# Kernel optimization log

Hardware: AMD Instinct MI355X
Metric: run time of the kernel (lower is better)

Reference implementation:

```python
import jax, jax.numpy as jnp
import numpy as np

B, DIM, IN_DIM, H, W = 4, 256, 128, 128, 128
DD = IN_DIM // 2          # down_dim = 64
HEADS = 8
BN_EPS = 1e-5


def conv2d(x, w, b=None, pad=0, dil=1):
    y = jax.lax.conv_general_dilated(
        x, w, window_strides=(1, 1),
        padding=[(pad, pad), (pad, pad)],
        rhs_dilation=(dil, dil),
        dimension_numbers=('NCHW', 'OIHW', 'NCHW'))
    if b is not None:
        y = y + b[None, :, None, None]
    return y


def bn_relu(x, s, o):
    # eval-mode BatchNorm2d with running_mean=0, running_var=1
    return jax.nn.relu(x * (s / np.sqrt(1.0 + BN_EPS))[None, :, None, None] + o[None, :, None, None])


def setup_inputs() -> dict:
    ks = iter(jax.random.split(jax.random.key(0), 80))

    def w(shape, sc=0.05):
        return sc * jax.random.normal(next(ks), shape, jnp.float32)

    def s(c):
        return 1.0 + 0.1 * jax.random.normal(next(ks), (c,), jnp.float32)

    def o(c):
        return 0.02 * jax.random.normal(next(ks), (c,), jnp.float32)

    d = {}
    d['x'] = jax.random.normal(next(ks), (B, DIM, H, W), jnp.float32)
    d['w_dc'] = w((IN_DIM, DIM, 3, 3)); d['b_dc'] = w((IN_DIM,)); d['s_dc'] = s(IN_DIM); d['o_dc'] = o(IN_DIM)
    d['w1'] = w((DD, IN_DIM, 1, 1)); d['b1'] = w((DD,)); d['s1'] = s(DD); d['o1'] = o(DD)
    d['w2'] = w((DD, DD, 3, 3)); d['b2'] = w((DD,)); d['s2'] = s(DD); d['o2'] = o(DD)
    d['w3'] = w((DD, DD, 3, 3)); d['b3'] = w((DD,)); d['s3'] = s(DD); d['o3'] = o(DD)
    d['w4'] = w((DD, DD, 3, 3)); d['b4'] = w((DD,)); d['s4'] = s(DD); d['o4'] = o(DD)
    d['w5'] = w((DD, IN_DIM, 1, 1)); d['b5'] = w((DD,)); d['s5'] = s(DD); d['o5'] = o(DD)
    d['temperature'] = jnp.ones((HEADS, 1, 1), jnp.float32)
    d['w_po'] = w((DD, 2 * DD, 1, 1))  # project_out, bias=False
    d['w_wa'] = w((DD // 16, DD, 1, 1)); d['b_wa'] = w((DD // 16,)); d['s_wa'] = s(DD // 16); d['o_wa'] = o(DD // 16)
    d['w_wb'] = w((DD, DD // 16, 1, 1)); d['b_wb'] = w((DD,))
    d['w_f'] = w((DD, 5 * DD, 1, 1)); d['b_f'] = w((DD,)); d['s_f'] = s(DD); d['o_f'] = o(DD)
    d['w_oa'] = w((DD // 2, DD, 3, 3)); d['b_oa'] = w((DD // 2,)); d['s_oa'] = s(DD // 2); d['o_oa'] = o(DD // 2)
    d['w_ob'] = w((1, DD // 2, 1, 1)); d['b_ob'] = w((1,))
    return d


def reference(x, w_dc, b_dc, s_dc, o_dc, w1, b1, s1, o1, w2, b2, s2, o2,
              w3, b3, s3, o3, w4, b4, s4, o4, w5, b5, s5, o5,
              temperature, w_po, w_wa, b_wa, s_wa, o_wa, w_wb, b_wb,
              w_f, b_f, s_f, o_f, w_oa, b_oa, s_oa, o_oa, w_ob, b_ob):

    def branch(c):
        b, ch, h, wd = c.shape
        f = jnp.fft.fft2(c)                                   # [b,ch,h,w] complex64 (q=k=v=tepqkv)
        qkv = f.reshape(b, HEADS, ch // HEADS, h * wd)        # v (unnormalized)
        n = jnp.sqrt(jnp.sum(jnp.square(jnp.abs(qkv)), axis=-1, keepdims=True))
        qn = qkv / jnp.maximum(n, 1e-12)                      # F.normalize(dim=-1); q == k
        attn = jnp.einsum('bhcn,bhdn->bhcd', qn, qn) * temperature
        # custom complex normalization: separate real/imag softmax
        attn = jax.lax.complex(jax.nn.softmax(attn.real, axis=-1),
                               jax.nn.softmax(attn.imag, axis=-1))
        of = jnp.abs(jnp.fft.ifft2(jnp.einsum('bhcd,bhdn->bhcn', attn, qkv)))  # ifft2 over (c, hw)
        of = of.reshape(b, ch, h, wd)
        g = jax.nn.sigmoid(conv2d(bn_relu(conv2d(f.real, w_wa, b_wa), s_wa, o_wa), w_wb, b_wb))
        ol = jnp.abs(jnp.fft.ifft2(g * f))                    # ifft2 over (h, w)
        return conv2d(jnp.concatenate([of, ol], axis=1), w_po) + c

    xd = bn_relu(conv2d(x, w_dc, b_dc, pad=1), s_dc, o_dc)
    c1 = bn_relu(conv2d(xd, w1, b1), s1, o1)
    c2 = bn_relu(conv2d(c1, w2, b2, pad=3, dil=3), s2, o2)
    F2 = branch(c2)
    c3 = bn_relu(conv2d(c1 + F2, w3, b3, pad=5, dil=5), s3, o3)
    F3 = branch(c3)
    c4 = bn_relu(conv2d(c1 + F3, w4, b4, pad=7, dil=7), s4, o4)
    F4 = branch(c4)
    # conv5: global avg pool -> 1x1 conv -> bilinear upsample of a 1x1 map == broadcast
    c5 = bn_relu(conv2d(jnp.mean(xd, axis=(2, 3), keepdims=True), w5, b5), s5, o5)
    c5 = jnp.broadcast_to(c5, (c5.shape[0], c5.shape[1], xd.shape[2], xd.shape[3]))
    fused = bn_relu(conv2d(jnp.concatenate([c1, F2, F3, F4, c5], axis=1), w_f, b_f), s_f, o_f)
    return conv2d(bn_relu(conv2d(fused, w_oa, b_oa, pad=1), s_oa, o_oa), w_ob, b_ob)
```

## Files before the change

### kernel.cpp

```cpp
#include <hip/hip_runtime.h>

#define S 16384
#define PI_F 3.14159265358979f

struct Ptrs { const float* p[43]; };

enum : int {
  O_SBDC=0, O_SB1=256, O_SB2=512, O_SB3=768, O_SB4=1024, O_SB5=1280,
  O_SBWA=1536, O_SBF=1792, O_SBOA=2048,
  O_M=2304, O_C5=2816, O_NRM=3072, O_GRAM=3328, O_ATT2=7424, O_BEFF=11520,
  O_WB=16384,
  O_PART=147456,
  O_H=180224,
  O_WP=442368,
  O_A=524288,
  O_FIN=8912896,
  O_CC=25690112,
  O_DRE=29884416, O_DIMG=34078720,
  O_ERE=38273024, O_EIM=42467328,
  O_G=46661632
};

typedef short bfrag __attribute__((ext_vector_type(8)));
typedef float ffrag __attribute__((ext_vector_type(4)));

__device__ __forceinline__ float bf2f(unsigned short u){
  union { unsigned int i; float f; } v; v.i = ((unsigned int)u) << 16; return v.f;
}
__device__ __forceinline__ unsigned short f2bf(float f){
  unsigned int x = __float_as_uint(f);
  unsigned int r = x + 0x7fffu + ((x >> 16) & 1u);
  return (unsigned short)(r >> 16);
}

__global__ void prep_sb_kernel(Ptrs P, float* ws){
  const float r = rsqrtf(1.0f + 1e-5f);
  int bi=0, si=0, oi=0, C=0, dst=0;
  switch (blockIdx.x){
    case 0: bi=2; si=3; oi=4; C=128; dst=O_SBDC; break;
    case 1: bi=6; si=7; oi=8; C=64; dst=O_SB1; break;
    case 2: bi=10; si=11; oi=12; C=64; dst=O_SB2; break;
    case 3: bi=14; si=15; oi=16; C=64; dst=O_SB3; break;
    case 4: bi=18; si=19; oi=20; C=64; dst=O_SB4; break;
    case 5: bi=22; si=23; oi=24; C=64; dst=O_SB5; break;
    case 6: bi=28; si=29; oi=30; C=4;  dst=O_SBWA; break;
    case 7: bi=34; si=35; oi=36; C=64; dst=O_SBF; break;
    default: bi=38; si=39; oi=40; C=32; dst=O_SBOA; break;
  }
  for (int c = threadIdx.x; c < C; c += 256){
    float bb = P.p[bi][c], ss = P.p[si][c], oo = P.p[oi][c];
    float sc = ss * r;
    ws[dst + c] = sc;
    ws[dst + C + c] = bb * sc + oo;
  }
}

__global__ __launch_bounds__(256) void xpad_kernel(const float* __restrict__ x,
    unsigned short* __restrict__ XT){
  int yy = blockIdx.x, b = blockIdx.y;
  long obase = ((long)(b*130) + yy) * (130L*256);
  int tid = threadIdx.x;
  if (yy == 0 || yy == 129){
    uint4 z; z.x=0; z.y=0; z.z=0; z.w=0;
    for (int i = tid; i < 130*256/8; i += 256)
      *(uint4*)(XT + obase + (long)i*8) = z;
    return;
  }
  __shared__ float LT[64][129];
  int y = yy - 1;
  for (int c0 = 0; c0 < 256; c0 += 64){
    for (int idx = tid; idx < 64*128; idx += 256){
      int ci = idx >> 7, xx = idx & 127;
      LT[ci][xx] = x[((long)(b*256 + c0 + ci)*128 + y)*128 + xx];
    }
    __syncthreads();
    for (int idx = tid; idx < 128*16; idx += 256){
      int xp = idx >> 4, c4 = (idx & 15)*4;
      ushort4 v;
      v.x = f2bf(LT[c4][xp]);   v.y = f2bf(LT[c4+1][xp]);
      v.z = f2bf(LT[c4+2][xp]); v.w = f2bf(LT[c4+3][xp]);
      *(ushort4*)(XT + obase + (long)(xp+1)*256 + c0 + c4) = v;
    }
    __syncthreads();
  }
  if (tid < 64){
    ushort4 z; z.x=0; z.y=0; z.z=0; z.w=0;
    *(ushort4*)(XT + obase + tid*4) = z;
    *(ushort4*)(XT + obase + 129L*256 + tid*4) = z;
  }
}

__global__ void wt_kernel(const float* __restrict__ w, unsigned short* __restrict__ WH,
    unsigned short* __restrict__ WL){
  for (int e = blockIdx.x*256 + threadIdx.x; e < 294912; e += gridDim.x*256){
    int c32 = e & 31, co = (e >> 5) & 127, kc = (e >> 12) & 7, sh = e >> 15;
    int ky = sh / 3, kx = sh - ky*3;
    int ci = kc*32 + c32;
    float v = w[((long)(co*256 + ci)*3 + ky)*3 + kx];
    unsigned short h = f2bf(v);
    WH[e] = h;
    WL[e] = f2bf(v - bf2f(h));
  }
}

__global__ void wtg_kernel(Ptrs P, unsigned short* __restrict__ WB){
  const float* w; int cout; long off;
  switch (blockIdx.y){
    case 0: w = P.p[9];  cout = 64; off = 0;      break;
    case 1: w = P.p[13]; cout = 64; off = 73728;  break;
    case 2: w = P.p[17]; cout = 64; off = 147456; break;
    default: w = P.p[37]; cout = 32; off = 221184; break;
  }
  int total = 576*cout;
  unsigned short* WH = WB + off;
  unsigned short* WL = WH + total;
  for (int e = blockIdx.x*256 + threadIdx.x; e < total; e += gridDim.x*256){
    int c32 = e & 31;
    int co = (e >> 5) & (cout - 1);
    int kc = (e / (32*cout)) & 1;
    int sh = e / (64*cout);
    int ky = sh/3, kx = sh - ky*3;
    int ci = kc*32 + c32;
    float v = w[((long)(co*64 + ci)*3 + ky)*3 + kx];
    unsigned short h = f2bf(v);
    WH[e] = h;
    WL[e] = f2bf(v - bf2f(h));
  }
}

__global__ void wtp_kernel(Ptrs P, unsigned short* __restrict__ WP){
  const float* w; int KC, wstr; long off;
  switch (blockIdx.y){
    case 0: w = P.p[5];  KC = 4; wstr = 128; off = 0;     break;
    case 1: w = P.p[26]; KC = 4; wstr = 128; off = 16384; break;
    default: w = P.p[33]; KC = 8; wstr = 320; off = 32768; break;
  }
  int total = KC*64*32;
  unsigned short* WH = WP + off;
  unsigned short* WL = WH + total;
  for (int e = blockIdx.x*256 + threadIdx.x; e < total; e += gridDim.x*256){
    int c32 = e & 31, co = (e >> 5) & 63, kc = e >> 11;
    float v = w[(long)co*wstr + kc*32 + c32];
    unsigned short h = f2bf(v);
    WH[e] = h;
    WL[e] = f2bf(v - bf2f(h));
  }
}

template<int DIL>
__global__ __launch_bounds__(256) void xpad64_kernel(const float* __restrict__ in1,
    const float* __restrict__ in2, long in_bs, unsigned short* __restrict__ XP){
  constexpr int TW = 128 + 2*DIL;
  int yy = blockIdx.x, b = blockIdx.y;
  long obase = (long)(b*TW + yy) * TW * 64;
  int tid = threadIdx.x;
  if (yy < DIL || yy >= 128 + DIL){
    uint4 z; z.x=0; z.y=0; z.z=0; z.w=0;
    for (int i = tid; i < TW*8; i += 256)
      *(uint4*)(XP + obase + (long)i*8) = z;
    return;
  }
  __shared__ float LT[64][129];
  int y = yy - DIL;
  const float* p1 = in1 + (long)b*in_bs + (long)y*128;
  const float* p2 = in2 ? in2 + (long)b*in_bs + (long)y*128 : nullptr;
  for (int idx = tid; idx < 64*128; idx += 256){
    int ci = idx >> 7, xx = idx & 127;
    float v = p1[(long)ci*S + xx];
    if (p2) v += p2[(long)ci*S + xx];
    LT[ci][xx] = v;
  }
  __syncthreads();
  for (int i = tid; i < 2*DIL*16; i += 256){
    int side = i / (DIL*16);
    int r = i - side*(DIL*16);
    int xcol = side ? (128 + DIL + (r >> 4)) : (r >> 4);
    ushort4 z; z.x=0; z.y=0; z.z=0; z.w=0;
    *(ushort4*)(XP + obase + (long)xcol*64 + (r & 15)*4) = z;
  }
  for (int idx = tid; idx < 128*16; idx += 256){
    int xp = idx >> 4, c4 = (idx & 15)*4;
    ushort4 v;
    v.x = f2bf(LT[c4][xp]);   v.y = f2bf(LT[c4+1][xp]);
    v.z = f2bf(LT[c4+2][xp]); v.w = f2bf(LT[c4+3][xp]);
    *(ushort4*)(XP + obase + (long)(xp + DIL)*64 + c4) = v;
  }
}

template<int DIL, int KC, int NBLK>
__global__ __launch_bounds__(256) void conv3x3_mfma_kernel(
    const unsigned short* __restrict__ XP,
    const unsigned short* __restrict__ WH, const unsigned short* __restrict__ WL,
    const float* __restrict__ scbi, float* __restrict__ out){
  constexpr int CIN = KC*32;
  constexpr int TW = 128 + 2*DIL;
  constexpr int STEPS = 9*KC;
  constexpr int MI = (NBLK == 64) ? 4 : 2;
  constexpr int LDA = 36;
  __shared__ unsigned short Als[128*LDA];
  __shared__ unsigned short BHs[NBLK*LDA];
  __shared__ unsigned short BLs[NBLK*LDA];
  int bid = blockIdx.x;
  int y = (bid & 7)*16 + ((bid >> 3) & 15);
  int b = (bid >> 7) & 3;
  int n2 = bid >> 9;
  int nb = gridDim.x >> 9; if (nb == 0) nb = 1;
  int coutTotal = nb * NBLK;
  int tid = threadIdx.x, wv = tid >> 6, lane = tid & 63;
  int mt0 = (NBLK == 64) ? (wv & 1)*4 : wv*2;
  int nt0 = (NBLK == 64) ? (wv >> 1)*2 : 0;
  ffrag acc[MI][2];
  #pragma unroll
  for (int i = 0; i < MI; i++)
    #pragma unroll
    for (int j = 0; j < 2; j++)
      #pragma unroll
      for (int r = 0; r < 4; r++) acc[i][j][r] = 0.f;

  int pixq = tid >> 2, qq = tid & 3;
  int kq = (lane >> 4)*8, rown = lane & 15;
  int wrA0 = pixq*LDA + qq*8;
  int wrA1 = (pixq + 64)*LDA + qq*8;
  int wrB  = (tid >> 2)*LDA + qq*8;

  uint4 A0, A1, BHr, BLr;
  {
    long abase = ((long)(b*TW + y)*TW)*CIN + qq*8;
    A0 = *(const uint4*)(XP + abase + (long)pixq*CIN);
    A1 = *(const uint4*)(XP + abase + (long)(pixq + 64)*CIN);
    long gw = (long)n2*NBLK*32;
    if (NBLK == 64 || tid < 128){
      BHr = *(const uint4*)(WH + gw + tid*8);
      BLr = *(const uint4*)(WL + gw + tid*8);
    }
  }
  for (int step = 0; step < STEPS; step++){
    __syncthreads();
    *(uint4*)&Als[wrA0] = A0;
    *(uint4*)&Als[wrA1] = A1;
    if (NBLK == 64 || tid < 128){
      *(uint4*)&BHs[wrB] = BHr;
      *(uint4*)&BLs[wrB] = BLr;
    }
    __syncthreads();
    if (step + 1 < STEPS){
      int s2 = step + 1;
      int sh = s2 / KC, kc = s2 - sh*KC;
      int ky = sh / 3, kx = sh - ky*3;
      long abase = ((long)(b*TW + y + ky*DIL)*TW + kx*DIL)*CIN + kc*32 + qq*8;
      A0 = *(const uint4*)(XP + abase + (long)pixq*CIN);
      A1 = *(const uint4*)(XP + abase + (long)(pixq + 64)*CIN);
      long gw = ((long)s2*coutTotal + n2*NBLK)*32;
      if (NBLK == 64 || tid < 128){
        BHr = *(const uint4*)(WH + gw + tid*8);
        BLr = *(const uint4*)(WL + gw + tid*8);
      }
    }
    bfrag af[MI], bhf[2], blf[2];
    #pragma unroll
    for (int i = 0; i < MI; i++)
      af[i] = *(const bfrag*)&Als[((mt0 + i)*16 + rown)*LDA + kq];
    #pragma unroll
    for (int j = 0; j < 2; j++){
      bhf[j] = *(const bfrag*)&BHs[((nt0 + j)*16 + rown)*LDA + kq];
      blf[j] = *(const bfrag*)&BLs[((nt0 + j)*16 + rown)*LDA + kq];
    }
    #pragma unroll
    for (int i = 0; i < MI; i++)
      #pragma unroll
      for (int j = 0; j < 2; j++){
        acc[i][j] = __builtin_amdgcn_mfma_f32_16x16x32_bf16(af[i], blf[j], acc[i][j], 0, 0, 0);
        acc[i][j] = __builtin_amdgcn_mfma_f32_16x16x32_bf16(af[i], bhf[j], acc[i][j], 0, 0, 0);
      }
  }
  #pragma unroll
  for (int i = 0; i < MI; i++){
    int pixel = (mt0 + i)*16 + (lane >> 4)*4;
    #pragma unroll
    for (int j = 0; j < 2; j++){
      int co = n2*NBLK + (nt0 + j)*16 + (lane & 15);
      float sc = scbi[co], bb = scbi[coutTotal + co];
      float* op = out + ((long)(b*coutTotal + co))*S + y*128 + pixel;
      #pragma unroll
      for (int r = 0; r < 4; r++)
        op[r] = fmaxf(acc[i][j][r]*sc + bb, 0.f);
    }
  }
}

template<int MODE, int KC, int BF16IN>
__global__ __launch_bounds__(256) void conv1x1_mfma_kernel(
    const void* __restrict__ inv, long in_bs,
    const unsigned short* __restrict__ WH, const unsigned short* __restrict__ WL,
    const float* __restrict__ scbi, const float* __restrict__ beff,
    const float* __restrict__ res, long res_bs,
    float* __restrict__ out, long out_bs){
  constexpr int LDA = 36;
  __shared__ unsigned short Als[128*LDA];
  __shared__ unsigned short BHs[64*LDA];
  __shared__ unsigned short BLs[64*LDA];
  int bid = blockIdx.x;
  int y = (bid & 7)*16 + ((bid >> 3) & 15);
  int b = bid >> 7;
  int tid = threadIdx.x, wv = tid >> 6, lane = tid & 63;
  int mt0 = (wv & 1)*4, nt0 = (wv >> 1)*2;
  ffrag acc[4][2];
  #pragma unroll
  for (int i = 0; i < 4; i++)
    #pragma unroll
    for (int j = 0; j < 2; j++)
      #pragma unroll
      for (int r = 0; r < 4; r++) acc[i][j][r] = 0.f;
  int pq = tid & 31, cg = tid >> 5;
  int kq = (lane >> 4)*8, rown = lane & 15;
  int wrB = (tid >> 2)*LDA + (tid & 3)*8;
  const float* ibf = (const float*)inv + (long)b*in_bs + y*128;
  const unsigned short* ibs = (const unsigned short*)inv + (long)b*in_bs + y*128;
  unsigned short a[16];
  uint4 BHr, BLr;
  #pragma unroll
  for (int cc = 0; cc < 4; cc++)
    #pragma unroll
    for (int i = 0; i < 4; i++){
      if (BF16IN) a[cc*4 + i] = ibs[(long)(cg*4 + cc)*S + pq + 32*i];
      else        a[cc*4 + i] = f2bf(ibf[(long)(cg*4 + cc)*S + pq + 32*i]);
    }
  BHr = *(const uint4*)(WH + tid*8);
  BLr = *(const uint4*)(WL + tid*8);
  for (int kc = 0; kc < KC; kc++){
    __syncthreads();
    #pragma unroll
    for (int i = 0; i < 4; i++){
      ushort4 v;
      v.x = a[0 + i];  v.y = a[4 + i];
      v.z = a[8 + i];  v.w = a[12 + i];
      *(ushort4*)&Als[(pq + 32*i)*LDA + cg*4] = v;
    }
    *(uint4*)&BHs[wrB] = BHr;
    *(uint4*)&BLs[wrB] = BLr;
    __syncthreads();
    if (kc + 1 < KC){
      #pragma unroll
      for (int cc = 0; cc < 4; cc++)
        #pragma unroll
        for (int i = 0; i < 4; i++){
          long off = (long)((kc + 1)*32 + cg*4 + cc)*S + pq + 32*i;
          if (BF16IN) a[cc*4 + i] = ibs[off];
          else        a[cc*4 + i] = f2bf(ibf[off]);
        }
      long gw = (long)(kc + 1)*2048;
      BHr = *(const uint4*)(WH + gw + tid*8);
      BLr = *(const uint4*)(WL + gw + tid*8);
    }
    bfrag af[4], bhf[2], blf[2];
    #pragma unroll
    for (int i = 0; i < 4; i++)
      af[i] = *(const bfrag*)&Als[((mt0 + i)*16 + rown)*LDA + kq];
    #pragma unroll
    for (int j = 0; j < 2; j++){
      bhf[j] = *(const bfrag*)&BHs[((nt0 + j)*16 + rown)*LDA + kq];
      blf[j] = *(const bfrag*)&BLs[((nt0 + j)*16 + rown)*LDA + kq];
    }
    #pragma unroll
    for (int i = 0; i < 4; i++)
      #pragma unroll
      for (int j = 0; j < 2; j++){
        acc[i][j] = __builtin_amdgcn_mfma_f32_16x16x32_bf16(af[i], blf[j], acc[i][j], 0, 0, 0);
        acc[i][j] = __builtin_amdgcn_mfma_f32_16x16x32_bf16(af[i], bhf[j], acc[i][j], 0, 0, 0);
      }
  }
  #pragma unroll
  for (int i = 0; i < 4; i++){
    int pixel = (mt0 + i)*16 + (lane >> 4)*4;
    #pragma unroll
    for (int j = 0; j < 2; j++){
      int co = (nt0 + j)*16 + (lane & 15);
      float* op = out + (long)b*out_bs + (long)co*S + y*128 + pixel;
      #pragma unroll
      for (int r = 0; r < 4; r++){
        float v = acc[i][j][r];
        if (MODE == 0){
          v = fmaxf(v*scbi[co] + scbi[64 + co], 0.f);
        } else if (MODE == 1){
          v += res[(long)b*res_bs + (long)co*S + y*128 + pixel + r];
        } else {
          v = fmaxf(v*scbi[co] + beff[b*64 + co], 0.f);
        }
        op[r] = v;
      }
    }
  }
}

__device__ __forceinline__ void fft128_mk_tw(float (&tws)[8], float (&twc)[8],
                                             float sign, int lane){
  float a0 = sign * (2.0f*PI_F/128.0f) * (float)lane;
  __sincosf(a0, &tws[0], &twc[0]);
  int i = 1;
  #pragma unroll
  for (int h = 32; h >= 1; h >>= 1, i++){
    int j = lane & (h - 1);
    float a = sign * (2.0f*PI_F/128.0f) * (float)(j * (64/h));
    __sincosf(a, &tws[i], &twc[i]);
  }
}

__device__ __forceinline__ void fft128(float& z0r, float& z0i, float& z1r, float& z1i,
    const float (&tws)[8], const float (&twc)[8], int lane){
  {
    float ar = z0r, ai = z0i, br = z1r, bi = z1i;
    z0r = ar + br; z0i = ai + bi;
    float dr = ar - br, di = ai - bi;
    float s = tws[0], c = twc[0];
    z1r = dr*c - di*s; z1i = dr*s + di*c;
  }
  int idx = 1;
  #pragma unroll
  for (int h = 32; h >= 1; h >>= 1, idx++){
    float s = tws[idx], c = twc[idx];
    bool up = (lane & h) != 0;
    float pr, pi, nr, ni;
    pr = __shfl_xor(z0r, h, 64); pi = __shfl_xor(z0i, h, 64);
    if (!up){ nr = z0r + pr; ni = z0i + pi; }
    else { float dr = pr - z0r, di = pi - z0i; nr = dr*c - di*s; ni = dr*s + di*c; }
    z0r = nr; z0i = ni;
    pr = __shfl_xor(z1r, h, 64); pi = __shfl_xor(z1i, h, 64);
    if (!up){ nr = z1r + pr; ni = z1i + pi; }
    else { float dr = pr - z1r, di = pi - z1i; nr = dr*c - di*s; ni = dr*s + di*c; }
    z1r = nr; z1i = ni;
  }
}

__global__ __launch_bounds__(256) void fft_rows_fwd_kernel(const float* __restrict__ in,
    unsigned short* __restrict__ outRe, unsigned short* __restrict__ outIm){
  int line = blockIdx.x*4 + (threadIdx.x >> 6);
  int lane = threadIdx.x & 63;
  float tws[8], twc[8];
  fft128_mk_tw(tws, twc, -1.0f, lane);
  long ib = (long)line * 128;
  float z0r = in[ib + lane], z0i = 0.f;
  float z1r = in[ib + lane + 64], z1i = 0.f;
  fft128(z0r, z0i, z1r, z1i, tws, twc, lane);
  int k = __brev(lane) >> 25;
  ushort2 vr; vr.x = f2bf(z0r); vr.y = f2bf(z1r);
  ushort2 vi; vi.x = f2bf(z0i); vi.y = f2bf(z1i);
  *(ushort2*)(outRe + ib + k) = vr;
  *(ushort2*)(outIm + ib + k) = vi;
}

template<int MODE>
__global__ __launch_bounds__(256) void fft_cols_kernel(
    const unsigned short* inRe, const unsigned short* inIm,
    unsigned short* outRe, unsigned short* outIm,
    const float* gate, const float* wb, const float* bwb){
  __shared__ float lre[128][17];
  __shared__ float lim[128][17];
  int plane = blockIdx.y;
  int cb = blockIdx.x * 16;
  int tid = threadIdx.x;
  long pbase = (long)plane * S;
  float w0=0.f, w1=0.f, w2=0.f, w3=0.f, bw=0.f;
  const float* Hb = nullptr;
  if (MODE == 1){
    int co = plane & 63;
    w0 = wb[co*4]; w1 = wb[co*4+1]; w2 = wb[co*4+2]; w3 = wb[co*4+3];
    bw = bwb[co];
    Hb = gate + (long)(plane >> 6) * 4 * S;
  }
  #pragma unroll
  for (int i = 0; i < 8; i++){
    int idx = tid + i*256;
    int r = idx >> 4, c = idx & 15;
    int pxl = r*128 + cb + c;
    long a = pbase + pxl;
    float re = bf2f(inRe[a]), im = bf2f(inIm[a]);
    if (MODE == 1){
      float hv = bw + w0*Hb[pxl] + w1*Hb[S + pxl] + w2*Hb[2*S + pxl] + w3*Hb[3*S + pxl];
      float g = 1.0f / (1.0f + __expf(-hv));
      re *= g; im *= g;
    }
    lre[r][c] = re; lim[r][c] = im;
  }
  __syncthreads();
  int wv = tid >> 6, lane = tid & 63;
  const float sign = (MODE == 0) ? -1.0f : 1.0f;
  float tws[8], twc[8];
  fft128_mk_tw(tws, twc, sign, lane);
  #pragma unroll
  for (int cc = 0; cc < 4; cc++){
    int c = wv*4 + cc;
    float z0r = lre[lane][c], z0i = lim[lane][c];
    float z1r = lre[lane + 64][c], z1i = lim[lane + 64][c];
    fft128(z0r, z0i, z1r, z1i, tws, twc, lane);
    int k = __brev(lane) >> 25;
    if (MODE == 2){
      int n2 = cb + c;
      float s, co;
      float a0 = (2.0f*PI_F/16384.0f) * (float)(n2 * k);
      __sincosf(a0, &s, &co);
      float t = z0r*co - z0i*s; z0i = z0r*s + z0i*co; z0r = t;
      float a1 = (2.0f*PI_F/16384.0f) * (float)(n2 * (k + 1));
      __sincosf(a1, &s, &co);
      t = z1r*co - z1i*s; z1i = z1r*s + z1i*co; z1r = t;
    }
    lre[k][c] = z0r;     lim[k][c] = z0i;
    lre[k + 1][c] = z1r; lim[k + 1][c] = z1i;
  }
  __syncthreads();
  #pragma unroll
  for (int i = 0; i < 8; i++){
    int idx = tid + i*256;
    int r = idx >> 4, c = idx & 15;
    long a = pbase + r*128 + cb + c;
    outRe[a] = f2bf(lre[r][c]); outIm[a] = f2bf(lim[r][c]);
  }
}

__global__ __launch_bounds__(256) void ifft_rows_abs_ol_kernel(
    const unsigned short* __restrict__ Ere, const unsigned short* __restrict__ Eim,
    unsigned short* __restrict__ AB){
  int line = blockIdx.x*4 + (threadIdx.x >> 6);
  int lane = threadIdx.x & 63;
  float tws[8], twc[8];
  fft128_mk_tw(tws, twc, 1.0f, lane);
  int plane = line >> 7, row = line & 127;
  long ib = (long)plane*S + row*128;
  float z0r = bf2f(Ere[ib + lane]), z0i = bf2f(Eim[ib + lane]);
  float z1r = bf2f(Ere[ib + lane + 64]), z1i = bf2f(Eim[ib + lane + 64]);
  fft128(z0r, z0i, z1r, z1i, tws, twc, lane);
  int b = plane >> 6, ch = plane & 63;
  unsigned short* out = AB + ((long)(b*128 + 64 + ch)) * S + row*128;
  int k = __brev(lane) >> 25;
  ushort2 v;
  v.x = f2bf(sqrtf(z0r*z0r + z0i*z0i) * (1.0f/16384.0f));
  v.y = f2bf(sqrtf(z1r*z1r + z1i*z1i) * (1.0f/16384.0f));
  *(ushort2*)(out + k) = v;
}

__global__ __launch_bounds__(256) void ifft_rows_abs_ofT_kernel(
    const unsigned short* __restrict__ Ere, const unsigned short* __restrict__ Eim,
    unsigned short* __restrict__ AB){
  __shared__ float T[128][17];
  int plane = blockIdx.y;
  int r0 = blockIdx.x * 16;
  int wv = threadIdx.x >> 6, lane = threadIdx.x & 63;
  float tws[8], twc[8];
  fft128_mk_tw(tws, twc, 1.0f, lane);
  #pragma unroll
  for (int i = 0; i < 4; i++){
    int rl = wv*4 + i;
    int row = r0 + rl;
    long ib = (long)plane*S + row*128;
    float z0r = bf2f(Ere[ib + lane]), z0i = bf2f(Eim[ib + lane]);
    float z1r = bf2f(Ere[ib + lane + 64]), z1i = bf2f(Eim[ib + lane + 64]);
    fft128(z0r, z0i, z1r, z1i, tws, twc, lane);
    int k = __brev(lane) >> 25;
    T[k][rl]     = sqrtf(z0r*z0r + z0i*z0i) * (1.0f/16384.0f);
    T[k + 1][rl] = sqrtf(z1r*z1r + z1i*z1i) * (1.0f/16384.0f);
  }
  __syncthreads();
  int b = plane >> 6, ch = plane & 63;
  unsigned short* out = AB + ((long)(b*128 + ch)) * S + r0;
  #pragma unroll
  for (int i = 0; i < 8; i++){
    int idx = threadIdx.x + i*256;
    int k2 = idx >> 4, rl = idx & 15;
    out[(long)k2*128 + rl] = f2bf(T[k2][rl]);
  }
}

__global__ __launch_bounds__(256) void gram_part_kernel(
    const unsigned short* __restrict__ Dre, const unsigned short* __restrict__ Dim,
    float* __restrict__ PART){
  int bh = blockIdx.x, slab = blockIdx.y;
  long base = (long)bh * 8 * S;
  int n0 = slab * 2048;
  float accr[36], acci[36], nsq[8];
  #pragma unroll
  for (int i = 0; i < 36; i++){ accr[i] = 0.f; acci[i] = 0.f; }
  #pragma unroll
  for (int i = 0; i < 8; i++) nsq[i] = 0.f;
  for (int it = 0; it < 8; it++){
    int n = n0 + it*256 + threadIdx.x;
    float xr[8], xi[8];
    #pragma unroll
    for (int c = 0; c < 8; c++){
      xr[c] = bf2f(Dre[base + (long)c*S + n]);
      xi[c] = bf2f(Dim[base + (long)c*S + n]);
      nsq[c] += xr[c]*xr[c] + xi[c]*xi[c];
    }
    int t = 0;
    #pragma unroll
    for (int c = 0; c < 8; c++)
      #pragma unroll
      for (int d = c; d < 8; d++){
        accr[t] += xr[c]*xr[d] - xi[c]*xi[d];
        acci[t] += xr[c]*xi[d] + xi[c]*xr[d];
        t++;
      }
  }
  __shared__ float red[4][80];
  int wv = threadIdx.x >> 6, lane = threadIdx.x & 63;
  #pragma unroll
  for (int i = 0; i < 80; i++){
    float v = (i < 36) ? accr[i] : (i < 72) ? acci[i - 36] : nsq[i - 72];
    #pragma unroll
    for (int o = 32; o; o >>= 1) v += __shfl_xor(v, o, 64);
    if (lane == 0) red[wv][i] = v;
  }
  __syncthreads();
  if (threadIdx.x < 80){
    int i = threadIdx.x;
    PART[(long)(bh*8 + slab)*80 + i] = red[0][i] + red[1][i] + red[2][i] + red[3][i];
  }
}

__global__ void attn2f_kernel(const float* __restrict__ PART,
    const float* __restrict__ temp, float* __restrict__ ATT2){
  __shared__ float ssum[80];
  __shared__ float sar[64], sai[64];
  int bh = blockIdx.x;
  int t = threadIdx.x;
  if (t < 80){
    float s = 0.f;
    for (int i = 0; i < 8; i++) s += PART[(long)(bh*8 + i)*80 + t];
    ssum[t] = s;
  }
  __syncthreads();
  if (t >= 64) return;
  int lane = t;
  int c = lane >> 3, d = lane & 7;
  int lo = min(c, d), hi = max(c, d);
  int t2 = lo*8 - lo*(lo - 1)/2 + (hi - lo);
  float nnc = fmaxf(sqrtf(ssum[72 + c]), 1e-12f);
  float nnd = fmaxf(sqrtf(ssum[72 + d]), 1e-12f);
  float inv = temp[bh & 7] / (nnc * nnd);
  float ar = ssum[t2] * inv, ai = ssum[36 + t2] * inv;
  float m = ar;
  m = fmaxf(m, __shfl_xor(m, 1, 64)); m = fmaxf(m, __shfl_xor(m, 2, 64)); m = fmaxf(m, __shfl_xor(m, 4, 64));
  float e = __expf(ar - m);
  float su = e;
  su += __shfl_xor(su, 1, 64); su += __shfl_xor(su, 2, 64); su += __shfl_xor(su, 4, 64);
  ar = e / su;
  m = ai;
  m = fmaxf(m, __shfl_xor(m, 1, 64)); m = fmaxf(m, __shfl_xor(m, 2, 64)); m = fmaxf(m, __shfl_xor(m, 4, 64));
  e = __expf(ai - m);
  su = e;
  su += __shfl_xor(su, 1, 64); su += __shfl_xor(su, 2, 64); su += __shfl_xor(su, 4, 64);
  ai = e / su;
  sar[lane] = ar; sai[lane] = ai;
  __syncthreads();
  const float ct[8] = {1.f, 0.70710678f, 0.f, -0.70710678f, -1.f, -0.70710678f, 0.f, 0.70710678f};
  const float st[8] = {0.f, 0.70710678f, 1.f, 0.70710678f, 0.f, -0.70710678f, -1.f, -0.70710678f};
  int cp = c;
  float sr = 0.f, si = 0.f;
  #pragma unroll
  for (int cc = 0; cc < 8; cc++){
    int k = (cc * cp) & 7;
    float a = sar[cc*8 + d], b2 = sai[cc*8 + d];
    sr += ct[k]*a - st[k]*b2;
    si += ct[k]*b2 + st[k]*a;
  }
  float2 v; v.x = sr * 0.125f; v.y = si * 0.125f;
  ((float2*)ATT2)[bh*64 + lane] = v;
}

__global__ __launch_bounds__(256) void apply_attn_kernel(
    const unsigned short* __restrict__ Dre, const unsigned short* __restrict__ Dim,
    const float* __restrict__ ATT2,
    unsigned short* __restrict__ Ere, unsigned short* __restrict__ Eim){
  int bh = blockIdx.y;
  int px = blockIdx.x*1024 + (threadIdx.x & 63)*4 + (threadIdx.x >> 6)*256;
  long base = (long)bh * 8 * S + px;
  float4 ar[8], ai[8];
  #pragma unroll
  for (int i = 0; i < 8; i++){
    ar[i].x = ar[i].y = ar[i].z = ar[i].w = 0.f;
    ai[i].x = ai[i].y = ai[i].z = ai[i].w = 0.f;
  }
  #pragma unroll
  for (int d = 0; d < 8; d++){
    ushort4 ur = *(const ushort4*)(Dre + base + (long)d*S);
    ushort4 ui = *(const ushort4*)(Dim + base + (long)d*S);
    float4 xr, xi;
    xr.x = bf2f(ur.x); xr.y = bf2f(ur.y); xr.z = bf2f(ur.z); xr.w = bf2f(ur.w);
    xi.x = bf2f(ui.x); xi.y = bf2f(ui.y); xi.z = bf2f(ui.z); xi.w = bf2f(ui.w);
    #pragma unroll
    for (int cp = 0; cp < 8; cp++){
      float wr = ATT2[bh*128 + (cp*8 + d)*2];
      float wi = ATT2[bh*128 + (cp*8 + d)*2 + 1];
      ar[cp].x += wr*xr.x - wi*xi.x;  ai[cp].x += wr*xi.x + wi*xr.x;
      ar[cp].y += wr*xr.y - wi*xi.y;  ai[cp].y += wr*xi.y + wi*xr.y;
      ar[cp].z += wr*xr.z - wi*xi.z;  ai[cp].z += wr*xi.z + wi*xr.z;
      ar[cp].w += wr*xr.w - wi*xi.w;  ai[cp].w += wr*xi.w + wi*xr.w;
    }
  }
  #pragma unroll
  for (int cp = 0; cp < 8; cp++){
    ushort4 vr, vi;
    vr.x = f2bf(ar[cp].x); vr.y = f2bf(ar[cp].y); vr.z = f2bf(ar[cp].z); vr.w = f2bf(ar[cp].w);
    vi.x = f2bf(ai[cp].x); vi.y = f2bf(ai[cp].y); vi.z = f2bf(ai[cp].z); vi.w = f2bf(ai[cp].w);
    *(ushort4*)(Ere + base + (long)cp*S) = vr;
    *(ushort4*)(Eim + base + (long)cp*S) = vi;
  }
}

__global__ __launch_bounds__(256) void gateh_kernel(const unsigned short* __restrict__ Dre,
    const float* __restrict__ wa, const float* __restrict__ sbwa, float* __restrict__ H){
  int b = blockIdx.y;
  int px = blockIdx.x*256 + threadIdx.x;
  long base = (long)b * 64 * S + px;
  float h0 = 0.f, h1 = 0.f, h2 = 0.f, h3 = 0.f;
  for (int ci = 0; ci < 64; ci++){
    float x = bf2f(Dre[base + (long)ci*S]);
    h0 += wa[ci]*x; h1 += wa[64 + ci]*x; h2 += wa[128 + ci]*x; h3 += wa[192 + ci]*x;
  }
  long ob = (long)b * 4 * S + px;
  H[ob]       = fmaxf(h0*sbwa[0] + sbwa[4], 0.f);
  H[ob + S]   = fmaxf(h1*sbwa[1] + sbwa[5], 0.f);
  H[ob + 2*S] = fmaxf(h2*sbwa[2] + sbwa[6], 0.f);
  H[ob + 3*S] = fmaxf(h3*sbwa[3] + sbwa[7], 0.f);
}

__global__ __launch_bounds__(256) void mean_kernel(const float* __restrict__ A, float* __restrict__ M){
  int p = blockIdx.x;
  long base = (long)p * S;
  float s = 0.f;
  for (int n = threadIdx.x; n < S; n += 256) s += A[base + n];
  #pragma unroll
  for (int o = 32; o; o >>= 1) s += __shfl_xor(s, o, 64);
  __shared__ float sm[4];
  if ((threadIdx.x & 63) == 0) sm[threadIdx.x >> 6] = s;
  __syncthreads();
  if (threadIdx.x == 0) M[p] = (sm[0] + sm[1] + sm[2] + sm[3]) * (1.0f/16384.0f);
}

__global__ void c5_kernel(const float* __restrict__ W5, const float* __restrict__ sb5,
    const float* __restrict__ M, float* __restrict__ C5){
  int t = threadIdx.x;
  if (t >= 256) return;
  int b = t >> 6, co = t & 63;
  float s = 0.f;
  for (int ci = 0; ci < 128; ci++) s += W5[co*128 + ci] * M[b*128 + ci];
  C5[t] = fmaxf(s * sb5[co] + sb5[64 + co], 0.f);
}

__global__ void beff_kernel(const float* __restrict__ WF, const float* __restrict__ sbf,
    const float* __restrict__ C5, float* __restrict__ BEFF){
  int t = threadIdx.x;
  if (t >= 256) return;
  int b = t >> 6, co = t & 63;
  float s = 0.f;
  for (int j = 0; j < 64; j++) s += WF[co*320 + 256 + j] * C5[b*64 + j];
  BEFF[t] = s * sbf[co] + sbf[64 + co];
}

__global__ __launch_bounds__(256) void ob_kernel(const float* __restrict__ Tin,
    const float* __restrict__ wob, const float* __restrict__ bob, float* __restrict__ out){
  int b = blockIdx.y;
  int px = blockIdx.x*1024 + (threadIdx.x & 63)*4 + (threadIdx.x >> 6)*256;
  float b0 = bob[0];
  float4 a; a.x = b0; a.y = b0; a.z = b0; a.w = b0;
  for (int ci = 0; ci < 32; ci++){
    float4 v = *(const float4*)(Tin + ((long)b*32 + ci)*S + px);
    float w = wob[ci];
    a.x += w*v.x; a.y += w*v.y; a.z += w*v.z; a.w += w*v.w;
  }
  *(float4*)(out + (long)b*S + px) = a;
}

extern "C" void kernel_launch(void* const* d_in, const int* in_sizes, int n_in,
                              void* d_out, int out_size, void* d_ws, size_t ws_size,
                              hipStream_t stream){
  float* ws = (float*)d_ws;
  Ptrs P;
  for (int i = 0; i < 43 && i < n_in; i++) P.p[i] = (const float*)d_in[i];
  float* out = (float*)d_out;

  float* A   = ws + O_A;
  float* FIN = ws + O_FIN;
  float* CC  = ws + O_CC;
  float* G   = ws + O_G;
  float* H   = ws + O_H;

  unsigned short* DRE16 = (unsigned short*)(ws + O_DRE);
  unsigned short* DIM16 = (unsigned short*)(ws + O_DIMG);
  unsigned short* ERE16 = (unsigned short*)(ws + O_ERE);
  unsigned short* EIM16 = (unsigned short*)(ws + O_EIM);
  unsigned short* AB    = (unsigned short*)(ws + O_A);

  unsigned short* XT  = (unsigned short*)(ws + O_DRE);
  unsigned short* WHd = (unsigned short*)(ws + O_CC);
  unsigned short* WLd = (unsigned short*)(ws + O_CC + 147456);
  unsigned short* WB  = (unsigned short*)(ws + O_WB);
  unsigned short* WP  = (unsigned short*)(ws + O_WP);
  unsigned short* XP  = (unsigned short*)(ws + O_ERE);

  prep_sb_kernel<<<dim3(9), dim3(256), 0, stream>>>(P, ws);
  xpad_kernel<<<dim3(130, 4), dim3(256), 0, stream>>>(P.p[0], XT);
  wt_kernel<<<dim3(128), dim3(256), 0, stream>>>(P.p[1], WHd, WLd);
  wtg_kernel<<<dim3(16, 4), dim3(256), 0, stream>>>(P, WB);
  wtp_kernel<<<dim3(8, 3), dim3(256), 0, stream>>>(P, WP);

  conv3x3_mfma_kernel<1,8,64><<<dim3(1024), dim3(256), 0, stream>>>(
      XT, WHd, WLd, ws + O_SBDC, A);

  mean_kernel<<<dim3(512), dim3(256), 0, stream>>>(A, ws + O_M);
  c5_kernel<<<dim3(1), dim3(256), 0, stream>>>(P.p[21], ws + O_SB5, ws + O_M, ws + O_C5);
  beff_kernel<<<dim3(1), dim3(256), 0, stream>>>(P.p[33], ws + O_SBF, ws + O_C5, ws + O_BEFF);

  conv1x1_mfma_kernel<0,4,0><<<dim3(512), dim3(256), 0, stream>>>(
      A, 128*S, WP, WP + 8192, ws + O_SB1, nullptr, nullptr, 0, FIN, 256*S);

  for (int k = 0; k < 3; k++){
    const float* sb = ws + (k == 0 ? O_SB2 : k == 1 ? O_SB3 : O_SB4);
    const float* in2 = (k == 0) ? nullptr : FIN + (long)(64*k)*S;
    unsigned short* wh = WB + (k == 0 ? 0 : k == 1 ? 73728 : 147456);
    if (k == 0){
      xpad64_kernel<3><<<dim3(134, 4), dim3(256), 0, stream>>>(FIN, in2, 256*S, XP);
      conv3x3_mfma_kernel<3,2,64><<<dim3(512), dim3(256), 0, stream>>>(
          XP, wh, wh + 36864, sb, CC);
    } else if (k == 1){
      xpad64_kernel<5><<<dim3(138, 4), dim3(256), 0, stream>>>(FIN, in2, 256*S, XP);
      conv3x3_mfma_kernel<5,2,64><<<dim3(512), dim3(256), 0, stream>>>(
          XP, wh, wh + 36864, sb, CC);
    } else {
      xpad64_kernel<7><<<dim3(142, 4), dim3(256), 0, stream>>>(FIN, in2, 256*S, XP);
      conv3x3_mfma_kernel<7,2,64><<<dim3(512), dim3(256), 0, stream>>>(
          XP, wh, wh + 36864, sb, CC);
    }

    fft_rows_fwd_kernel<<<dim3(8192), dim3(256), 0, stream>>>(CC, DRE16, DIM16);
    fft_cols_kernel<0><<<dim3(8, 256), dim3(256), 0, stream>>>(
        DRE16, DIM16, DRE16, DIM16, nullptr, nullptr, nullptr);
    gram_part_kernel<<<dim3(32, 8), dim3(256), 0, stream>>>(DRE16, DIM16, ws + O_PART);
    attn2f_kernel<<<dim3(32), dim3(128), 0, stream>>>(ws + O_PART, P.p[25], ws + O_ATT2);
    gateh_kernel<<<dim3(64, 4), dim3(256), 0, stream>>>(DRE16, P.p[27], ws + O_SBWA, H);
    fft_cols_kernel<1><<<dim3(8, 256), dim3(256), 0, stream>>>(
        DRE16, DIM16, ERE16, EIM16, H, P.p[31], P.p[32]);
    ifft_rows_abs_ol_kernel<<<dim3(8192), dim3(256), 0, stream>>>(ERE16, EIM16, AB);
    apply_attn_kernel<<<dim3(16, 32), dim3(256), 0, stream>>>(DRE16, DIM16, ws + O_ATT2, ERE16, EIM16);
    fft_cols_kernel<2><<<dim3(8, 256), dim3(256), 0, stream>>>(
        ERE16, EIM16, ERE16, EIM16, nullptr, nullptr, nullptr);
    ifft_rows_abs_ofT_kernel<<<dim3(8, 256), dim3(256), 0, stream>>>(ERE16, EIM16, AB);
    conv1x1_mfma_kernel<1,4,1><<<dim3(512), dim3(256), 0, stream>>>(
        AB, 128*S, WP + 16384, WP + 24576, nullptr, nullptr, CC, 64*S,
        FIN + (long)(64*(k + 1))*S, 256*S);
  }

  conv1x1_mfma_kernel<2,8,0><<<dim3(512), dim3(256), 0, stream>>>(
      FIN, 256*S, WP + 32768, WP + 49152, ws + O_SBF, ws + O_BEFF, nullptr, 0, CC, 64*S);
  xpad64_kernel<1><<<dim3(130, 4), dim3(256), 0, stream>>>(CC, nullptr, 64*S, XP);
  conv3x3_mfma_kernel<1,2,32><<<dim3(512), dim3(256), 0, stream>>>(
      XP, WB + 221184, WB + 221184 + 18432, ws + O_SBOA, G);
  ob_kernel<<<dim3(16, 4), dim3(256), 0, stream>>>(G, P.p[41], P.p[42], out);
}
```

Before: 984.3 us.

## Fuse channel mean into conv epilogue and attention mixing into inverse FFT

The channel mean is now computed in the first conv3x3 epilogue with shuffle reductions and atomicAdd into a buffer that prep_sb zeroes. This removes the separate mean pass over the 128-channel activation. The c5 and beff kernels merge into one launch. The apply_attn kernel is removed: the column FFT now runs on the raw spectrum, and the 8x8 complex attention mix is applied inside the inverse row FFT, relying on linearity to commute the mix with the column transform. This drops one full read-write pass over the complex planes but reads eight input planes per output plane, and the FFT grids are flattened to 1D with plane as the fast index.

```diff
diff --git a/kernel.cpp b/kernel.cpp
--- a/kernel.cpp
+++ b/kernel.cpp
@@ -45,7 +45,10 @@
     case 5: bi=22; si=23; oi=24; C=64; dst=O_SB5; break;
     case 6: bi=28; si=29; oi=30; C=4;  dst=O_SBWA; break;
     case 7: bi=34; si=35; oi=36; C=64; dst=O_SBF; break;
-    default: bi=38; si=39; oi=40; C=32; dst=O_SBOA; break;
+    case 8: bi=38; si=39; oi=40; C=32; dst=O_SBOA; break;
+    default:
+      for (int c = threadIdx.x; c < 512; c += 256) ws[O_M + c] = 0.f;
+      return;
   }
   for (int c = threadIdx.x; c < C; c += 256){
     float bb = P.p[bi][c], ss = P.p[si][c], oo = P.p[oi][c];
@@ -187,11 +190,11 @@
   }
 }
 
-template<int DIL, int KC, int NBLK>
+template<int DIL, int KC, int NBLK, int FM>
 __global__ __launch_bounds__(256) void conv3x3_mfma_kernel(
     const unsigned short* __restrict__ XP,
     const unsigned short* __restrict__ WH, const unsigned short* __restrict__ WL,
-    const float* __restrict__ scbi, float* __restrict__ out){
+    const float* __restrict__ scbi, float* __restrict__ out, float* __restrict__ Msum){
   constexpr int CIN = KC*32;
   constexpr int TW = 128 + 2*DIL;
   constexpr int STEPS = 9*KC;
@@ -273,6 +276,7 @@
         acc[i][j] = __builtin_amdgcn_mfma_f32_16x16x32_bf16(af[i], bhf[j], acc[i][j], 0, 0, 0);
       }
   }
+  float ps0 = 0.f, ps1 = 0.f;
   #pragma unroll
   for (int i = 0; i < MI; i++){
     int pixel = (mt0 + i)*16 + (lane >> 4)*4;
@@ -282,8 +286,23 @@
       float sc = scbi[co], bb = scbi[coutTotal + co];
       float* op = out + ((long)(b*coutTotal + co))*S + y*128 + pixel;
       #pragma unroll
-      for (int r = 0; r < 4; r++)
-        op[r] = fmaxf(acc[i][j][r]*sc + bb, 0.f);
+      for (int r = 0; r < 4; r++){
+        float v = fmaxf(acc[i][j][r]*sc + bb, 0.f);
+        op[r] = v;
+        if (FM){ if (j == 0) ps0 += v; else ps1 += v; }
+      }
+    }
+  }
+  if (FM){
+    #pragma unroll
+    for (int j = 0; j < 2; j++){
+      float v = ((j == 0) ? ps0 : ps1) * (1.0f/16384.0f);
+      v += __shfl_xor(v, 16, 64);
+      v += __shfl_xor(v, 32, 64);
+      if ((lane >> 4) == 0){
+        int co = n2*NBLK + (nt0 + j)*16 + (lane & 15);
+        atomicAdd(&Msum[b*coutTotal + co], v);
+      }
     }
   }
 }
@@ -455,8 +474,9 @@
     const float* gate, const float* wb, const float* bwb){
   __shared__ float lre[128][17];
   __shared__ float lim[128][17];
-  int plane = blockIdx.y;
-  int cb = blockIdx.x * 16;
+  int bid = blockIdx.x;
+  int plane = bid & 255;
+  int cb = (bid >> 8) * 16;
   int tid = threadIdx.x;
   long pbase = (long)plane * S;
   float w0=0.f, w1=0.f, w2=0.f, w3=0.f, bw=0.f;
@@ -539,20 +559,35 @@
 
 __global__ __launch_bounds__(256) void ifft_rows_abs_ofT_kernel(
     const unsigned short* __restrict__ Ere, const unsigned short* __restrict__ Eim,
-    unsigned short* __restrict__ AB){
+    const float* __restrict__ ATT2, unsigned short* __restrict__ AB){
   __shared__ float T[128][17];
   int plane = blockIdx.y;
   int r0 = blockIdx.x * 16;
   int wv = threadIdx.x >> 6, lane = threadIdx.x & 63;
+  int bh = plane >> 3, cp = plane & 7;
+  long gbase = (long)(plane & ~7) * S;
+  float wr[8], wi[8];
+  #pragma unroll
+  for (int d = 0; d < 8; d++){
+    wr[d] = ATT2[bh*128 + (cp*8 + d)*2];
+    wi[d] = ATT2[bh*128 + (cp*8 + d)*2 + 1];
+  }
   float tws[8], twc[8];
   fft128_mk_tw(tws, twc, 1.0f, lane);
   #pragma unroll
   for (int i = 0; i < 4; i++){
     int rl = wv*4 + i;
     int row = r0 + rl;
-    long ib = (long)plane*S + row*128;
-    float z0r = bf2f(Ere[ib + lane]), z0i = bf2f(Eim[ib + lane]);
-    float z1r = bf2f(Ere[ib + lane + 64]), z1i = bf2f(Eim[ib + lane + 64]);
+    long ib = gbase + row*128;
+    float z0r = 0.f, z0i = 0.f, z1r = 0.f, z1i = 0.f;
+    #pragma unroll
+    for (int d = 0; d < 8; d++){
+      long a = ib + (long)d*S;
+      float xr0 = bf2f(Ere[a + lane]),      xi0 = bf2f(Eim[a + lane]);
+      float xr1 = bf2f(Ere[a + lane + 64]), xi1 = bf2f(Eim[a + lane + 64]);
+      z0r += wr[d]*xr0 - wi[d]*xi0;  z0i += wr[d]*xi0 + wi[d]*xr0;
+      z1r += wr[d]*xr1 - wi[d]*xi1;  z1i += wr[d]*xi1 + wi[d]*xr1;
+    }
     fft128(z0r, z0i, z1r, z1i, tws, twc, lane);
     int k = __brev(lane) >> 25;
     T[k][rl]     = sqrtf(z0r*z0r + z0i*z0i) * (1.0f/16384.0f);
@@ -665,46 +700,6 @@
   ((float2*)ATT2)[bh*64 + lane] = v;
 }
 
-__global__ __launch_bounds__(256) void apply_attn_kernel(
-    const unsigned short* __restrict__ Dre, const unsigned short* __restrict__ Dim,
-    const float* __restrict__ ATT2,
-    unsigned short* __restrict__ Ere, unsigned short* __restrict__ Eim){
-  int bh = blockIdx.y;
-  int px = blockIdx.x*1024 + (threadIdx.x & 63)*4 + (threadIdx.x >> 6)*256;
-  long base = (long)bh * 8 * S + px;
-  float4 ar[8], ai[8];
-  #pragma unroll
-  for (int i = 0; i < 8; i++){
-    ar[i].x = ar[i].y = ar[i].z = ar[i].w = 0.f;
-    ai[i].x = ai[i].y = ai[i].z = ai[i].w = 0.f;
-  }
-  #pragma unroll
-  for (int d = 0; d < 8; d++){
-    ushort4 ur = *(const ushort4*)(Dre + base + (long)d*S);
-    ushort4 ui = *(const ushort4*)(Dim + base + (long)d*S);
-    float4 xr, xi;
-    xr.x = bf2f(ur.x); xr.y = bf2f(ur.y); xr.z = bf2f(ur.z); xr.w = bf2f(ur.w);
-    xi.x = bf2f(ui.x); xi.y = bf2f(ui.y); xi.z = bf2f(ui.z); xi.w = bf2f(ui.w);
-    #pragma unroll
-    for (int cp = 0; cp < 8; cp++){
-      float wr = ATT2[bh*128 + (cp*8 + d)*2];
-      float wi = ATT2[bh*128 + (cp*8 + d)*2 + 1];
-      ar[cp].x += wr*xr.x - wi*xi.x;  ai[cp].x += wr*xi.x + wi*xr.x;
-      ar[cp].y += wr*xr.y - wi*xi.y;  ai[cp].y += wr*xi.y + wi*xr.y;
-      ar[cp].z += wr*xr.z - wi*xi.z;  ai[cp].z += wr*xi.z + wi*xr.z;
-      ar[cp].w += wr*xr.w - wi*xi.w;  ai[cp].w += wr*xi.w + wi*xr.w;
-    }
-  }
-  #pragma unroll
-  for (int cp = 0; cp < 8; cp++){
-    ushort4 vr, vi;
-    vr.x = f2bf(ar[cp].x); vr.y = f2bf(ar[cp].y); vr.z = f2bf(ar[cp].z); vr.w = f2bf(ar[cp].w);
-    vi.x = f2bf(ai[cp].x); vi.y = f2bf(ai[cp].y); vi.z = f2bf(ai[cp].z); vi.w = f2bf(ai[cp].w);
-    *(ushort4*)(Ere + base + (long)cp*S) = vr;
-    *(ushort4*)(Eim + base + (long)cp*S) = vi;
-  }
-}
-
 __global__ __launch_bounds__(256) void gateh_kernel(const unsigned short* __restrict__ Dre,
     const float* __restrict__ wa, const float* __restrict__ sbwa, float* __restrict__ H){
   int b = blockIdx.y;
@@ -722,37 +717,19 @@
   H[ob + 3*S] = fmaxf(h3*sbwa[3] + sbwa[7], 0.f);
 }
 
-__global__ __launch_bounds__(256) void mean_kernel(const float* __restrict__ A, float* __restrict__ M){
-  int p = blockIdx.x;
-  long base = (long)p * S;
-  float s = 0.f;
-  for (int n = threadIdx.x; n < S; n += 256) s += A[base + n];
-  #pragma unroll
-  for (int o = 32; o; o >>= 1) s += __shfl_xor(s, o, 64);
-  __shared__ float sm[4];
-  if ((threadIdx.x & 63) == 0) sm[threadIdx.x >> 6] = s;
-  __syncthreads();
-  if (threadIdx.x == 0) M[p] = (sm[0] + sm[1] + sm[2] + sm[3]) * (1.0f/16384.0f);
-}
-
-__global__ void c5_kernel(const float* __restrict__ W5, const float* __restrict__ sb5,
-    const float* __restrict__ M, float* __restrict__ C5){
+__global__ void c5beff_kernel(const float* __restrict__ W5, const float* __restrict__ sb5,
+    const float* __restrict__ WF, const float* __restrict__ sbf,
+    const float* __restrict__ M, float* __restrict__ BEFF){
+  __shared__ float C5s[256];
   int t = threadIdx.x;
-  if (t >= 256) return;
   int b = t >> 6, co = t & 63;
   float s = 0.f;
   for (int ci = 0; ci < 128; ci++) s += W5[co*128 + ci] * M[b*128 + ci];
-  C5[t] = fmaxf(s * sb5[co] + sb5[64 + co], 0.f);
-}
-
-__global__ void beff_kernel(const float* __restrict__ WF, const float* __restrict__ sbf,
-    const float* __restrict__ C5, float* __restrict__ BEFF){
-  int t = threadIdx.x;
-  if (t >= 256) return;
-  int b = t >> 6, co = t & 63;
-  float s = 0.f;
-  for (int j = 0; j < 64; j++) s += WF[co*320 + 256 + j] * C5[b*64 + j];
-  BEFF[t] = s * sbf[co] + sbf[64 + co];
+  C5s[t] = fmaxf(s * sb5[co] + sb5[64 + co], 0.f);
+  __syncthreads();
+  float s2 = 0.f;
+  for (int j = 0; j < 64; j++) s2 += WF[co*320 + 256 + j] * C5s[b*64 + j];
+  BEFF[t] = s2 * sbf[co] + sbf[64 + co];
 }
 
 __global__ __launch_bounds__(256) void ob_kernel(const float* __restrict__ Tin,
@@ -796,18 +773,17 @@
   unsigned short* WP  = (unsigned short*)(ws + O_WP);
   unsigned short* XP  = (unsigned short*)(ws + O_ERE);
 
-  prep_sb_kernel<<<dim3(9), dim3(256), 0, stream>>>(P, ws);
+  prep_sb_kernel<<<dim3(10), dim3(256), 0, stream>>>(P, ws);
   xpad_kernel<<<dim3(130, 4), dim3(256), 0, stream>>>(P.p[0], XT);
   wt_kernel<<<dim3(128), dim3(256), 0, stream>>>(P.p[1], WHd, WLd);
   wtg_kernel<<<dim3(16, 4), dim3(256), 0, stream>>>(P, WB);
   wtp_kernel<<<dim3(8, 3), dim3(256), 0, stream>>>(P, WP);
 
-  conv3x3_mfma_kernel<1,8,64><<<dim3(1024), dim3(256), 0, stream>>>(
-      XT, WHd, WLd, ws + O_SBDC, A);
-
-  mean_kernel<<<dim3(512), dim3(256), 0, stream>>>(A, ws + O_M);
-  c5_kernel<<<dim3(1), dim3(256), 0, stream>>>(P.p[21], ws + O_SB5, ws + O_M, ws + O_C5);
-  beff_kernel<<<dim3(1), dim3(256), 0, stream>>>(P.p[33], ws + O_SBF, ws + O_C5, ws + O_BEFF);
+  conv3x3_mfma_kernel<1,8,64,1><<<dim3(1024), dim3(256), 0, stream>>>(
+      XT, WHd, WLd, ws + O_SBDC, A, ws + O_M);
+
+  c5beff_kernel<<<dim3(1), dim3(256), 0, stream>>>(
+      P.p[21], ws + O_SB5, P.p[33], ws + O_SBF, ws + O_M, ws + O_BEFF);
 
   conv1x1_mfma_kernel<0,4,0><<<dim3(512), dim3(256), 0, stream>>>(
       A, 128*S, WP, WP + 8192, ws + O_SB1, nullptr, nullptr, 0, FIN, 256*S);
@@ -818,31 +794,31 @@
     unsigned short* wh = WB + (k == 0 ? 0 : k == 1 ? 73728 : 147456);
     if (k == 0){
       xpad64_kernel<3><<<dim3(134, 4), dim3(256), 0, stream>>>(FIN, in2, 256*S, XP);
-      conv3x3_mfma_kernel<3,2,64><<<dim3(512), dim3(256), 0, stream>>>(
-          XP, wh, wh + 36864, sb, CC);
+      conv3x3_mfma_kernel<3,2,64,0><<<dim3(512), dim3(256), 0, stream>>>(
+          XP, wh, wh + 36864, sb, CC, nullptr);
     } else if (k == 1){
       xpad64_kernel<5><<<dim3(138, 4), dim3(256), 0, stream>>>(FIN, in2, 256*S, XP);
-      conv3x3_mfma_kernel<5,2,64><<<dim3(512), dim3(256), 0, stream>>>(
-          XP, wh, wh + 36864, sb, CC);
+      conv3x3_mfma_kernel<5,2,64,0><<<dim3(512), dim3(256), 0, stream>>>(
+          XP, wh, wh + 36864, sb, CC, nullptr);
     } else {
       xpad64_kernel<7><<<dim3(142, 4), dim3(256), 0, stream>>>(FIN, in2, 256*S, XP);
-      conv3x3_mfma_kernel<7,2,64><<<dim3(512), dim3(256), 0, stream>>>(
-          XP, wh, wh + 36864, sb, CC);
+      conv3x3_mfma_kernel<7,2,64,0><<<dim3(512), dim3(256), 0, stream>>>(
+          XP, wh, wh + 36864, sb, CC, nullptr);
     }
 
     fft_rows_fwd_kernel<<<dim3(8192), dim3(256), 0, stream>>>(CC, DRE16, DIM16);
-    fft_cols_kernel<0><<<dim3(8, 256), dim3(256), 0, stream>>>(
+    fft_cols_kernel<0><<<dim3(2048), dim3(256), 0, stream>>>(
         DRE16, DIM16, DRE16, DIM16, nullptr, nullptr, nullptr);
     gram_part_kernel<<<dim3(32, 8), dim3(256), 0, stream>>>(DRE16, DIM16, ws + O_PART);
     attn2f_kernel<<<dim3(32), dim3(128), 0, stream>>>(ws + O_PART, P.p[25], ws + O_ATT2);
     gateh_kernel<<<dim3(64, 4), dim3(256), 0, stream>>>(DRE16, P.p[27], ws + O_SBWA, H);
-    fft_cols_kernel<1><<<dim3(8, 256), dim3(256), 0, stream>>>(
+    fft_cols_kernel<1><<<dim3(2048), dim3(256), 0, stream>>>(
         DRE16, DIM16, ERE16, EIM16, H, P.p[31], P.p[32]);
     ifft_rows_abs_ol_kernel<<<dim3(8192), dim3(256), 0, stream>>>(ERE16, EIM16, AB);
-    apply_attn_kernel<<<dim3(16, 32), dim3(256), 0, stream>>>(DRE16, DIM16, ws + O_ATT2, ERE16, EIM16);
-    fft_cols_kernel<2><<<dim3(8, 256), dim3(256), 0, stream>>>(
-        ERE16, EIM16, ERE16, EIM16, nullptr, nullptr, nullptr);
-    ifft_rows_abs_ofT_kernel<<<dim3(8, 256), dim3(256), 0, stream>>>(ERE16, EIM16, AB);
+    fft_cols_kernel<2><<<dim3(2048), dim3(256), 0, stream>>>(
+        DRE16, DIM16, ERE16, EIM16, nullptr, nullptr, nullptr);
+    ifft_rows_abs_ofT_kernel<<<dim3(8, 256), dim3(256), 0, stream>>>(
+        ERE16, EIM16, ws + O_ATT2, AB);
     conv1x1_mfma_kernel<1,4,1><<<dim3(512), dim3(256), 0, stream>>>(
         AB, 128*S, WP + 16384, WP + 24576, nullptr, nullptr, CC, 64*S,
         FIN + (long)(64*(k + 1))*S, 256*S);
@@ -851,7 +827,7 @@
   conv1x1_mfma_kernel<2,8,0><<<dim3(512), dim3(256), 0, stream>>>(
       FIN, 256*S, WP + 32768, WP + 49152, ws + O_SBF, ws + O_BEFF, nullptr, 0, CC, 64*S);
   xpad64_kernel<1><<<dim3(130, 4), dim3(256), 0, stream>>>(CC, nullptr, 64*S, XP);
-  conv3x3_mfma_kernel<1,2,32><<<dim3(512), dim3(256), 0, stream>>>(
-      XP, WB + 221184, WB + 221184 + 18432, ws + O_SBOA, G);
+  conv3x3_mfma_kernel<1,2,32,0><<<dim3(512), dim3(256), 0, stream>>>(
+      XP, WB + 221184, WB + 221184 + 18432, ws + O_SBOA, G, nullptr);
   ob_kernel<<<dim3(16, 4), dim3(256), 0, stream>>>(G, P.p[41], P.p[42], out);
 }
```

Result: slower. 1.048 ms (+6.5%).
